# Kernel tuning notes

Measured on AMD Instinct MI355X. Metric: run time of the kernel, lower is better.

Reference implementation:

```python
import jax, jax.numpy as jnp
import numpy as np

B, S, HID = 4, 1024, 4096
NH, NKV, HD = 32, 8, 128
FF = 11008
EPS = 1e-6
THETA = 10000.0


def rms_norm(x, w, eps=EPS):
    v = jnp.mean(jnp.square(x), axis=-1, keepdims=True)
    return x * jax.lax.rsqrt(v + eps) * w


def rotate_half(x):
    x1, x2 = jnp.split(x, 2, axis=-1)
    return jnp.concatenate([-x2, x1], axis=-1)


def rope_cos_sin(position_ids, head_dim=HD, theta=THETA):
    inv_freq = 1.0 / (theta ** (jnp.arange(0, head_dim, 2, dtype=jnp.float32) / head_dim))
    freqs = position_ids.astype(jnp.float32)[..., None] * inv_freq  # [B,S,HD/2]
    emb = jnp.concatenate([freqs, freqs], axis=-1)  # [B,S,HD]
    return jnp.cos(emb)[:, None, :, :], jnp.sin(emb)[:, None, :, :]  # [B,1,S,HD]


def setup_inputs() -> dict:
    key = jax.random.key(0)
    ks = jax.random.split(key, 9)
    sc = 0.02
    pos = jnp.tile(jnp.arange(S, dtype=jnp.int64 if jax.config.jax_enable_x64 else jnp.int32)[None, :], (B, 1))
    causal = jnp.tril(jnp.ones((S, S), dtype=bool))
    mask = jnp.where(causal, 0.0, -1e9).astype(jnp.float32)[None, None]  # [1,1,S,S]
    return {
        "hidden_states": jax.random.normal(ks[0], (B * S, HID), jnp.float32),
        "position_ids": pos,
        "attn_mask": mask,
        "Wq": jax.random.normal(ks[1], (HID, NH * HD), jnp.float32) * sc,
        "Wk": jax.random.normal(ks[2], (HID, NKV * HD), jnp.float32) * sc,
        "Wv": jax.random.normal(ks[3], (HID, NKV * HD), jnp.float32) * sc,
        "Wo": jax.random.normal(ks[4], (NH * HD, HID), jnp.float32) * sc,
        "ln1_w": jnp.ones((HID,), jnp.float32),
        "ln2_w": jnp.ones((HID,), jnp.float32),
        "w_gate": jax.random.normal(ks[5], (HID, FF), jnp.float32) * sc,
        "w_up": jax.random.normal(ks[6], (HID, FF), jnp.float32) * sc,
        "w_down": jax.random.normal(ks[7], (FF, HID), jnp.float32) * sc,
    }


def reference(hidden_states, position_ids, attn_mask, Wq, Wk, Wv, Wo, ln1_w, ln2_w, w_gate, w_up, w_down):
    residual = hidden_states
    h = rms_norm(hidden_states, ln1_w)

    # QKV projections on flat tokens, then reshape per train partition
    q = (h @ Wq).reshape(B, S, NH, HD).transpose(0, 2, 1, 3)     # [B,NH,S,HD]
    k = (h @ Wk).reshape(B, S, NKV, HD).transpose(0, 2, 1, 3)    # [B,NKV,S,HD]
    v = (h @ Wv).reshape(B, S, NKV, HD).transpose(0, 2, 1, 3)

    cos, sin = rope_cos_sin(position_ids)
    q = q * cos + rotate_half(q) * sin
    k = k * cos + rotate_half(k) * sin

    n_rep = NH // NKV
    k = jnp.repeat(k, n_rep, axis=1)  # [B,NH,S,HD]
    v = jnp.repeat(v, n_rep, axis=1)

    scores = jnp.einsum('bhqd,bhkd->bhqk', q, k) / np.sqrt(HD)
    scores = scores + attn_mask
    # softmax in fp32 as in the source
    probs = jax.nn.softmax(scores.astype(jnp.float32), axis=-1).astype(q.dtype)
    attn = jnp.einsum('bhqk,bhkd->bhqd', probs, v)               # [B,NH,S,HD]
    attn = attn.transpose(0, 2, 1, 3).reshape(B * S, NH * HD)
    h = attn @ Wo

    h = residual + h
    residual = h
    h2 = rms_norm(h, ln2_w)
    mlp = (jax.nn.silu(h2 @ w_gate) * (h2 @ w_up)) @ w_down
    return residual + mlp
```

## Files before the change

### kernel.cpp

```cpp
#include <hip/hip_runtime.h>

#define DEVINL __device__ __forceinline__

typedef unsigned short u16;
typedef __attribute__((ext_vector_type(8))) short bf16x8;
typedef __attribute__((ext_vector_type(4))) float f32x4;
typedef __attribute__((ext_vector_type(4))) unsigned short u16x4;


DEVINL float bf2f(u16 u) { union { unsigned i; float f; } x; x.i = ((unsigned)u) << 16; return x.f; }
DEVINL u16 f2bf(float f) {
  union { float f; unsigned i; } x; x.f = f;
  unsigned r = x.i + 0x7fffu + ((x.i >> 16) & 1u);
  return (u16)(r >> 16);
}

DEVINL void async16(u16* lds, const u16* g) {
  __builtin_amdgcn_global_load_lds((const __attribute__((address_space(1))) unsigned*)g,
                                   (__attribute__((address_space(3))) unsigned*)lds, 16, 0, 0);
}

__global__ __launch_bounds__(256) void conv_t(const float* __restrict__ in,
                                              u16* __restrict__ out, int K, int N) {
  __shared__ float tile[64][65];
  int k0 = blockIdx.y << 6, n0 = blockIdx.x << 6;
  int t = threadIdx.x;
  int r = t >> 4, c4 = (t & 15) << 2;
  #pragma unroll
  for (int it = 0; it < 4; it++) {
    int row = r + it*16;
    f32x4 v = *(const f32x4*)(in + (size_t)(k0 + row)*N + n0 + c4);
    tile[row][c4+0] = v[0]; tile[row][c4+1] = v[1];
    tile[row][c4+2] = v[2]; tile[row][c4+3] = v[3];
  }
  __syncthreads();
  #pragma unroll
  for (int it = 0; it < 4; it++) {
    int nrow = r + it*16;
    u16x4 ov;
    #pragma unroll
    for (int e = 0; e < 4; e++) ov[e] = f2bf(tile[c4+e][nrow]);
    *(u16x4*)(out + (size_t)(n0 + nrow)*K + k0 + c4) = ov;
  }
}

__global__ __launch_bounds__(256) void rmsnorm_kernel(const float* __restrict__ x,
                                                      const float* __restrict__ w,
                                                      u16* __restrict__ out) {
  int row = blockIdx.x, t = threadIdx.x;
  const float* xr = x + (size_t)row * 4096;
  f32x4 v[4];
  float ss = 0.f;
  #pragma unroll
  for (int i = 0; i < 4; i++) {
    v[i] = *(const f32x4*)(xr + (t + 256*i)*4);
    ss += v[i][0]*v[i][0] + v[i][1]*v[i][1] + v[i][2]*v[i][2] + v[i][3]*v[i][3];
  }
  #pragma unroll
  for (int d = 1; d < 64; d <<= 1) ss += __shfl_xor(ss, d, 64);
  __shared__ float ps[4];
  if ((t & 63) == 0) ps[t >> 6] = ss;
  __syncthreads();
  float scale = rsqrtf((ps[0]+ps[1]+ps[2]+ps[3]) * (1.f/4096.f) + 1e-6f);
  #pragma unroll
  for (int i = 0; i < 4; i++) {
    f32x4 wv = *(const f32x4*)(w + (t + 256*i)*4);
    u16x4 o;
    #pragma unroll
    for (int e = 0; e < 4; e++) o[e] = f2bf(v[i][e] * scale * wv[e]);
    *(u16x4*)(out + (size_t)row*4096 + (t + 256*i)*4) = o;
  }
}

__global__ __launch_bounds__(256) void rope_kernel(u16* __restrict__ q, u16* __restrict__ k) {
  int tok = blockIdx.x;
  int s = tok & 1023;
  __shared__ float cs[64], sn[64];
  int t = threadIdx.x;
  if (t < 64) {
    float inv = __expf(-(float)t * 0.14391156934f);
    float ang = (float)s * inv;
    cs[t] = cosf(ang); sn[t] = sinf(ang);
  }
  __syncthreads();
  const float qscale = 0.08838834764831845f;
  size_t qbase = (size_t)tok * 4096;
  #pragma unroll
  for (int it = 0; it < 8; it++) {
    int item = t + it*256; int h = item >> 6, j = item & 63;
    size_t i0 = qbase + h*128 + j;
    float x1 = bf2f(q[i0]), x2 = bf2f(q[i0+64]);
    float c = cs[j], si = sn[j];
    q[i0]    = f2bf((x1*c - x2*si) * qscale);
    q[i0+64] = f2bf((x2*c + x1*si) * qscale);
  }
  size_t kbase = (size_t)tok * 1024;
  #pragma unroll
  for (int it = 0; it < 2; it++) {
    int item = t + it*256; int h = item >> 6, j = item & 63;
    size_t i0 = kbase + h*128 + j;
    float x1 = bf2f(k[i0]), x2 = bf2f(k[i0+64]);
    float c = cs[j], si = sn[j];
    k[i0]    = f2bf(x1*c - x2*si);
    k[i0+64] = f2bf(x2*c + x1*si);
  }
}

__global__ __launch_bounds__(256) void vtrans(const u16* __restrict__ v, u16* __restrict__ vt) {
  __shared__ u16 tile[32][33];
  int bh = blockIdx.z; int b = bh >> 3, kvh = bh & 7;
  int d0 = blockIdx.x << 5, s0 = blockIdx.y << 5;
  int tx = threadIdx.x, ty = threadIdx.y;
  for (int r = ty; r < 32; r += 8)
    tile[r][tx] = v[(size_t)(b*1024 + s0 + r)*1024 + kvh*128 + d0 + tx];
  __syncthreads();
  for (int r = ty; r < 32; r += 8)
    vt[(size_t)((b*8 + kvh)*128 + d0 + r)*1024 + s0 + tx] = tile[tx][r];
}

template<int EPI>
__global__ __launch_bounds__(256, 2) void gemm_bt(
    const u16* __restrict__ A, const u16* __restrict__ Bt,
    void* __restrict__ Cv, const float* __restrict__ resid,
    const u16* __restrict__ gate, int M, int N, int K) {
  __shared__ u16 As[128*64];
  __shared__ u16 Bs[128*64];
  int nwg = gridDim.x;
  int bid = (int)blockIdx.x;
  int cpx = nwg >> 3;
  int swz = (bid & 7) * cpx + (bid >> 3);
  int mt = M >> 7;
  int m0 = (swz % mt) << 7;
  int n0 = (swz / mt) << 7;
  int tid = threadIdx.x;
  int lane = tid & 63, wave = tid >> 6;
  int wm = wave >> 1, wn = wave & 1;

  f32x4 acc[4][4];
  f32x4 zero = {0.f, 0.f, 0.f, 0.f};
  #pragma unroll
  for (int i = 0; i < 4; i++)
    #pragma unroll
    for (int j = 0; j < 4; j++) acc[i][j] = zero;

  int arow[4], acolb[4];
  #pragma unroll
  for (int i = 0; i < 4; i++) {
    int c = i*256 + tid;
    arow[i]  = c >> 3;
    acolb[i] = ((c & 7) * 16) ^ ((arow[i] & 7) << 4);
  }

  int nsteps = K >> 6;
  for (int t = 0; t < nsteps; t++) {
    int k0 = t << 6;
    #pragma unroll
    for (int i = 0; i < 4; i++) {
      async16(As + i*2048 + wave*512, A  + (size_t)(m0 + arow[i])*K + k0 + (acolb[i] >> 1));
      async16(Bs + i*2048 + wave*512, Bt + (size_t)(n0 + arow[i])*K + k0 + (acolb[i] >> 1));
    }
    __syncthreads();
    #pragma unroll
    for (int ks = 0; ks < 2; ks++) {
      bf16x8 af[4], bfr[4];
      int c2 = (ks*32 + (lane >> 4)*8) * 2;
      #pragma unroll
      for (int mf = 0; mf < 4; mf++) {
        int r = wm*64 + mf*16 + (lane & 15);
        af[mf] = *(const bf16x8*)(As + r*64 + ((c2 ^ ((r & 7) << 4)) >> 1));
      }
      #pragma unroll
      for (int nf = 0; nf < 4; nf++) {
        int r = wn*64 + nf*16 + (lane & 15);
        bfr[nf] = *(const bf16x8*)(Bs + r*64 + ((c2 ^ ((r & 7) << 4)) >> 1));
      }
      #pragma unroll
      for (int mf = 0; mf < 4; mf++)
        #pragma unroll
        for (int nf = 0; nf < 4; nf++)
          acc[mf][nf] = __builtin_amdgcn_mfma_f32_16x16x32_bf16(af[mf], bfr[nf], acc[mf][nf], 0, 0, 0);
    }
    __syncthreads();
  }

  #pragma unroll
  for (int mf = 0; mf < 4; mf++)
    #pragma unroll
    for (int nf = 0; nf < 4; nf++)
      #pragma unroll
      for (int j = 0; j < 4; j++) {
        int rr = m0 + wm*64 + mf*16 + (lane >> 4)*4 + j;
        int cc = n0 + wn*64 + nf*16 + (lane & 15);
        size_t idx = (size_t)rr * N + cc;
        float v = acc[mf][nf][j];
        if constexpr (EPI == 0) {
          ((u16*)Cv)[idx] = f2bf(v);
        } else if constexpr (EPI == 1) {
          ((float*)Cv)[idx] = v + resid[idx];
        } else {
          float g = bf2f(gate[idx]);
          float sg = g / (1.f + __expf(-g));
          ((u16*)Cv)[idx] = f2bf(sg * v);
        }
      }
}

#define SB0() __builtin_amdgcn_sched_barrier(0)
#define MIDBAR() do { SB0(); __builtin_amdgcn_s_barrier(); \
  asm volatile("s_waitcnt lgkmcnt(0)" ::: "memory"); SB0(); } while (0)
#define MFMAQ2(qm, qn, afr, bq) do { \
  __builtin_amdgcn_s_setprio(1); \
  _Pragma("unroll") for (int mf_ = 0; mf_ < 4; mf_++) \
  _Pragma("unroll") for (int nf_ = 0; nf_ < 2; nf_++) \
  _Pragma("unroll") for (int ks_ = 0; ks_ < 2; ks_++) \
    acc[(qm)*4+mf_][(qn)*2+nf_] = __builtin_amdgcn_mfma_f32_16x16x32_bf16( \
        afr[mf_][ks_], bq[nf_][ks_], acc[(qm)*4+mf_][(qn)*2+nf_], 0, 0, 0); \
  __builtin_amdgcn_s_setprio(0); } while (0)

template<int EPI>
__global__ __launch_bounds__(512, 2) void gemm256(
    const u16* __restrict__ A, const u16* __restrict__ Bt,
    void* __restrict__ Cv, const float* __restrict__ resid,
    const u16* __restrict__ gate, int M, int N, int K) {
  extern __shared__ u16 lds[];
  int nwg = gridDim.x, bid = (int)blockIdx.x;
  int cpx = nwg >> 3;
  int swz = (bid & 7) * cpx + (bid >> 3);
  int mt = M >> 8;
  int m0 = (swz % mt) << 8;
  int n0 = (swz / mt) << 8;
  int tid = threadIdx.x, lane = tid & 63, wave = tid >> 6;
  int wm = wave >> 2, wn = wave & 3;

  f32x4 acc[8][4];
  f32x4 zero = {0.f, 0.f, 0.f, 0.f};
  #pragma unroll
  for (int i = 0; i < 8; i++)
    #pragma unroll
    for (int j = 0; j < 4; j++) acc[i][j] = zero;

  int sCol = ((lane & 7) ^ (lane >> 3)) << 3;
  int aRow = ((wave >> 2)*128) + (wave & 3)*16 + (lane >> 3);
  int bRow = ((wave >> 1)*64)  + (wave & 1)*16 + (lane >> 3);
  const u16* gA = A  + (size_t)(m0 + aRow) * K + sCol;
  const u16* gB = Bt + (size_t)(n0 + bRow) * K + sCol;
  size_t K8 = (size_t)8 * K, K32 = (size_t)32 * K, K64 = (size_t)64 * K;

  int rA = lane & 15;
  int acol0 = (((lane >> 4)    ) ^ (rA & 7)) << 3;
  int acol1 = (((lane >> 4) + 4) ^ (rA & 7)) << 3;

  bf16x8 af[4][2], b0[2][2], b1[2][2];

  auto stageAq = [&](int buf, int qm, int k0) {
    u16* d = lds + buf*32768 + qm*8192 + wave*1024;
    const u16* s = gA + (size_t)qm*K64 + k0;
    async16(d, s); async16(d + 512, s + K8);
  };
  auto stageBq = [&](int buf, int qn, int k0) {
    u16* d = lds + buf*32768 + 16384 + qn*8192 + wave*1024;
    const u16* s = gB + (size_t)qn*K32 + k0;
    async16(d, s); async16(d + 512, s + K8);
  };
  auto loadAq = [&](int buf, int qm) {
    const u16* base = lds + buf*32768 + qm*8192 + wm*4096 + rA*64;
    #pragma unroll
    for (int mf = 0; mf < 4; mf++) {
      af[mf][0] = *(const bf16x8*)(base + mf*1024 + acol0);
      af[mf][1] = *(const bf16x8*)(base + mf*1024 + acol1);
    }
  };
  auto loadBq = [&](int buf, int qn, bf16x8 (&bq)[2][2]) {
    const u16* base = lds + buf*32768 + 16384 + qn*8192 + wn*2048 + rA*64;
    #pragma unroll
    for (int nf = 0; nf < 2; nf++) {
      bq[nf][0] = *(const bf16x8*)(base + nf*1024 + acol0);
      bq[nf][1] = *(const bf16x8*)(base + nf*1024 + acol1);
    }
  };

  int nt = K >> 6;
  stageAq(0, 0, 0); stageBq(0, 0, 0); stageBq(0, 1, 0); stageAq(0, 1, 0);
  SB0();
  asm volatile("s_waitcnt vmcnt(4)" ::: "memory");
  SB0();
  __builtin_amdgcn_s_barrier();

  for (int k = 0; k < nt; k++) {
    int buf = k & 1, nbuf = buf ^ 1;
    bool pre = (k + 1) < nt;
    int k1 = (k + 1) << 6;
    loadAq(buf, 0); loadBq(buf, 0, b0);
    if (pre) stageAq(nbuf, 0, k1);
    MIDBAR();
    MFMAQ2(0, 0, af, b0);
    SB0();
    if (pre) asm volatile("s_waitcnt vmcnt(4)" ::: "memory");
    else     asm volatile("s_waitcnt vmcnt(2)" ::: "memory");
    SB0(); __builtin_amdgcn_s_barrier();
    loadBq(buf, 1, b1);
    if (pre) stageBq(nbuf, 0, k1);
    MIDBAR();
    MFMAQ2(0, 1, af, b1);
    SB0();
    if (pre) asm volatile("s_waitcnt vmcnt(4)" ::: "memory");
    else     asm volatile("s_waitcnt vmcnt(0)" ::: "memory");
    SB0(); __builtin_amdgcn_s_barrier();
    loadAq(buf, 1);
    if (pre) stageBq(nbuf, 1, k1);
    MIDBAR();
    MFMAQ2(1, 0, af, b0);
    SB0(); __builtin_amdgcn_s_barrier();
    if (pre) stageAq(nbuf, 1, k1);
    MIDBAR();
    MFMAQ2(1, 1, af, b1);
    SB0();
    if (pre) asm volatile("s_waitcnt vmcnt(4)" ::: "memory");
    SB0(); __builtin_amdgcn_s_barrier();
  }

  #pragma unroll
  for (int mf = 0; mf < 8; mf++)
    #pragma unroll
    for (int nf = 0; nf < 4; nf++)
      #pragma unroll
      for (int j = 0; j < 4; j++) {
        int rr = m0 + wm*128 + mf*16 + (lane >> 4)*4 + j;
        int cc = n0 + wn*64 + nf*16 + (lane & 15);
        size_t idx = (size_t)rr * N + cc;
        float v = acc[mf][nf][j];
        if constexpr (EPI == 0) {
          ((u16*)Cv)[idx] = f2bf(v);
        } else if constexpr (EPI == 1) {
          ((float*)Cv)[idx] = v + resid[idx];
        } else {
          float g = bf2f(gate[idx]);
          float sg = g / (1.f + __expf(-g));
          ((u16*)Cv)[idx] = f2bf(sg * v);
        }
      }
}

__global__ __launch_bounds__(256, 2) void attn_kernel(
    const u16* __restrict__ q, const u16* __restrict__ k,
    const u16* __restrict__ vt, u16* __restrict__ out) {
  __shared__ u16 Ks[64*128];
  __shared__ u16 Vs[128*64];
  __shared__ u16 Ps[4*16*64];
  int bid = blockIdx.x;
  int qt = bid & 15;
  int h  = (bid >> 4) & 31;
  int b  = bid >> 9;
  int kvh = h >> 2;
  int tid = threadIdx.x, lane = tid & 63, wave = tid >> 6;
  int q0 = qt << 6;

  bf16x8 qf[4];
  {
    const u16* qb_ = q + (size_t)(b*1024 + q0 + wave*16 + (lane & 15))*4096 + h*128 + (lane >> 4)*8;
    #pragma unroll
    for (int ks = 0; ks < 4; ks++) qf[ks] = *(const bf16x8*)(qb_ + ks*32);
  }
  f32x4 o[8];
  f32x4 zero = {0.f,0.f,0.f,0.f};
  #pragma unroll
  for (int i = 0; i < 8; i++) o[i] = zero;
  float m[4] = {-1e30f,-1e30f,-1e30f,-1e30f};
  float l[4] = {0.f,0.f,0.f,0.f};

  int kr[4], kc[4], vr[4], vc[4];
  #pragma unroll
  for (int i = 0; i < 4; i++) {
    int c = i*256 + tid;
    kr[i] = c >> 4; kc[i] = ((c & 15)*16) ^ ((kr[i] & 7) << 4);
    vr[i] = c >> 3; vc[i] = ((c & 7)*16)  ^ ((vr[i] & 7) << 4);
  }

  for (int t = 0; t <= qt; t++) {
    int kv0 = t << 6;
    #pragma unroll
    for (int i = 0; i < 4; i++) {
      async16(Ks + i*2048 + wave*512, k  + (size_t)(b*1024 + kv0 + kr[i])*1024 + kvh*128 + (kc[i] >> 1));
      async16(Vs + i*2048 + wave*512, vt + (size_t)((b*8 + kvh)*128 + vr[i])*1024 + kv0 + (vc[i] >> 1));
    }
    __syncthreads();

    f32x4 s[4];
    #pragma unroll
    for (int nf = 0; nf < 4; nf++) {
      s[nf] = zero;
      #pragma unroll
      for (int ks = 0; ks < 4; ks++) {
        int r = nf*16 + (lane & 15);
        int c2 = (ks*32 + (lane >> 4)*8)*2;
        bf16x8 kf = *(const bf16x8*)(Ks + r*128 + ((c2 ^ ((r & 7) << 4)) >> 1));
        s[nf] = __builtin_amdgcn_mfma_f32_16x16x32_bf16(qf[ks], kf, s[nf], 0, 0, 0);
      }
    }
    if (t == qt) {
      #pragma unroll
      for (int nf = 0; nf < 4; nf++)
        #pragma unroll
        for (int j = 0; j < 4; j++) {
          int cc = nf*16 + (lane & 15);
          int rr = wave*16 + (lane >> 4)*4 + j;
          if (cc > rr) s[nf][j] = -1e30f;
        }
    }
    #pragma unroll
    for (int j = 0; j < 4; j++) {
      float mx = fmaxf(fmaxf(s[0][j], s[1][j]), fmaxf(s[2][j], s[3][j]));
      #pragma unroll
      for (int d = 1; d < 16; d <<= 1) mx = fmaxf(mx, __shfl_xor(mx, d, 64));
      float mn = fmaxf(m[j], mx);
      float f = __expf(m[j] - mn);
      m[j] = mn;
      float ssum = 0.f;
      #pragma unroll
      for (int nf = 0; nf < 4; nf++) {
        float p = __expf(s[nf][j] - mn);
        s[nf][j] = p; ssum += p;
      }
      #pragma unroll
      for (int d = 1; d < 16; d <<= 1) ssum += __shfl_xor(ssum, d, 64);
      l[j] = l[j]*f + ssum;
      #pragma unroll
      for (int nf = 0; nf < 8; nf++) o[nf][j] *= f;
    }
    #pragma unroll
    for (int nf = 0; nf < 4; nf++)
      #pragma unroll
      for (int j = 0; j < 4; j++) {
        int rr = (lane >> 4)*4 + j;
        int cb = ((nf*16 + (lane & 15))*2) ^ ((rr & 7) << 4);
        Ps[wave*1024 + rr*64 + (cb >> 1)] = f2bf(s[nf][j]);
      }
    #pragma unroll
    for (int ks2 = 0; ks2 < 2; ks2++) {
      int mr = lane & 15;
      int c2 = (ks2*32 + (lane >> 4)*8)*2;
      bf16x8 pa = *(const bf16x8*)(Ps + wave*1024 + mr*64 + ((c2 ^ ((mr & 7) << 4)) >> 1));
      #pragma unroll
      for (int nf = 0; nf < 8; nf++) {
        int d = nf*16 + (lane & 15);
        bf16x8 vf = *(const bf16x8*)(Vs + d*64 + ((c2 ^ ((d & 7) << 4)) >> 1));
        o[nf] = __builtin_amdgcn_mfma_f32_16x16x32_bf16(pa, vf, o[nf], 0, 0, 0);
      }
    }
    __syncthreads();
  }

  float inv[4];
  #pragma unroll
  for (int j = 0; j < 4; j++) inv[j] = 1.f / l[j];
  u16* ob = out + (size_t)(b*1024 + q0 + wave*16)*4096 + h*128;
  #pragma unroll
  for (int nf = 0; nf < 8; nf++)
    #pragma unroll
    for (int j = 0; j < 4; j++) {
      int rr = (lane >> 4)*4 + j;
      int cc = nf*16 + (lane & 15);
      ob[(size_t)rr*4096 + cc] = f2bf(o[nf][j] * inv[j]);
    }
}

extern "C" void kernel_launch(void* const* d_in, const int* in_sizes, int n_in,
                              void* d_out, int out_size, void* d_ws, size_t ws_size,
                              hipStream_t stream) {
  (void)in_sizes; (void)n_in; (void)out_size;
  const float* hidden = (const float*)d_in[0];
  const float* Wq  = (const float*)d_in[3];
  const float* Wk  = (const float*)d_in[4];
  const float* Wv  = (const float*)d_in[5];
  const float* Wo  = (const float*)d_in[6];
  const float* ln1 = (const float*)d_in[7];
  const float* ln2 = (const float*)d_in[8];
  const float* Wg  = (const float*)d_in[9];
  const float* Wu  = (const float*)d_in[10];
  const float* Wd  = (const float*)d_in[11];
  float* out = (float*)d_out;

  char* ws = (char*)d_ws;
  size_t off = 0;
  auto alloc = [&](size_t b) { char* p = ws + off; off += (b + 4095) & ~(size_t)4095; return p; };
  u16*  W1   = (u16*)alloc(90177536);
  u16*  h1   = (u16*)alloc(33554432);
  u16*  qb   = (u16*)alloc(33554432);
  u16*  kb   = (u16*)alloc(8388608);
  u16*  vb   = (u16*)alloc(8388608);
  u16*  vtb  = (u16*)alloc(8388608);
  float* hmid = (float*)alloc(67108864);
  u16*  gb   = (u16*)alloc(90177536);
  if (off > ws_size) return;

  u16* wqT = W1;
  u16* wkT = W1 + 16777216;
  u16* wvT = wkT + 4194304;

  hipFuncSetAttribute((const void*)gemm256<0>, hipFuncAttributeMaxDynamicSharedMemorySize, 131072);
  hipFuncSetAttribute((const void*)gemm256<1>, hipFuncAttributeMaxDynamicSharedMemorySize, 131072);
  hipFuncSetAttribute((const void*)gemm256<2>, hipFuncAttributeMaxDynamicSharedMemorySize, 131072);

  dim3 blk(256);
  conv_t<<<dim3(64, 64),  blk, 0, stream>>>(Wq, wqT, 4096, 4096);
  conv_t<<<dim3(16, 64),  blk, 0, stream>>>(Wk, wkT, 4096, 1024);
  conv_t<<<dim3(16, 64),  blk, 0, stream>>>(Wv, wvT, 4096, 1024);
  rmsnorm_kernel<<<4096, blk, 0, stream>>>(hidden, ln1, h1);
  gemm256<0><<<256, 512, 131072, stream>>>(h1, wqT, qb, nullptr, nullptr, 4096, 4096, 4096);
  gemm_bt<0><<<256, blk, 0, stream>>>(h1, wkT, kb, nullptr, nullptr, 4096, 1024, 4096);
  gemm_bt<0><<<256, blk, 0, stream>>>(h1, wvT, vb, nullptr, nullptr, 4096, 1024, 4096);
  rope_kernel<<<4096, blk, 0, stream>>>(qb, kb);
  vtrans<<<dim3(4, 32, 32), dim3(32, 8), 0, stream>>>(vb, vtb);
  attn_kernel<<<2048, blk, 0, stream>>>(qb, kb, vtb, h1);
  conv_t<<<dim3(64, 64), blk, 0, stream>>>(Wo, W1, 4096, 4096);
  gemm256<1><<<256, 512, 131072, stream>>>(h1, W1, hmid, hidden, nullptr, 4096, 4096, 4096);
  rmsnorm_kernel<<<4096, blk, 0, stream>>>(hmid, ln2, qb);
  conv_t<<<dim3(172, 64), blk, 0, stream>>>(Wg, W1, 4096, 11008);
  gemm256<0><<<688, 512, 131072, stream>>>(qb, W1, gb, nullptr, nullptr, 4096, 11008, 4096);
  conv_t<<<dim3(172, 64), blk, 0, stream>>>(Wu, W1, 4096, 11008);
  gemm256<2><<<688, 512, 131072, stream>>>(qb, W1, gb, nullptr, gb, 4096, 11008, 4096);
  conv_t<<<dim3(64, 172), blk, 0, stream>>>(Wd, W1, 11008, 4096);
  gemm256<1><<<256, 512, 131072, stream>>>(gb, W1, out, hmid, nullptr, 4096, 4096, 11008);
}
```

Baseline: 1.836 ms.

## Overlap LDS fragment loads with MFMA via double-buffered A registers in gemm256

Restructures the 256x256 GEMM main loop so LDS-to-register fragment loads for the next quadrant (and the next K-tile's first A/B quadrant) are issued before the current MFMA block. Partial lgkmcnt waits replace the full lgkmcnt(0) after each barrier. A second A-fragment register set is added so loads and math can overlap, and two barriers per iteration are dropped. This aims to hide LDS read latency behind matrix-core work. The cost is more register pressure under launch_bounds(512,2) and fragile hand-counted wait counts.

After: 1.819 ms. About the same (-0.9%).

```diff
diff --git a/kernel.cpp b/kernel.cpp
--- a/kernel.cpp
+++ b/kernel.cpp
@@ -206,15 +206,13 @@
 }
 
 #define SB0() __builtin_amdgcn_sched_barrier(0)
-#define MIDBAR() do { SB0(); __builtin_amdgcn_s_barrier(); \
-  asm volatile("s_waitcnt lgkmcnt(0)" ::: "memory"); SB0(); } while (0)
-#define MFMAQ2(qm, qn, afr, bq) do { \
+#define MFMAQ2(qm, qn, AF, BQ) do { \
   __builtin_amdgcn_s_setprio(1); \
   _Pragma("unroll") for (int mf_ = 0; mf_ < 4; mf_++) \
   _Pragma("unroll") for (int nf_ = 0; nf_ < 2; nf_++) \
   _Pragma("unroll") for (int ks_ = 0; ks_ < 2; ks_++) \
     acc[(qm)*4+mf_][(qn)*2+nf_] = __builtin_amdgcn_mfma_f32_16x16x32_bf16( \
-        afr[mf_][ks_], bq[nf_][ks_], acc[(qm)*4+mf_][(qn)*2+nf_], 0, 0, 0); \
+        AF[mf_][ks_], BQ[nf_][ks_], acc[(qm)*4+mf_][(qn)*2+nf_], 0, 0, 0); \
   __builtin_amdgcn_s_setprio(0); } while (0)
 
 template<int EPI>
@@ -250,7 +248,7 @@
   int acol0 = (((lane >> 4)    ) ^ (rA & 7)) << 3;
   int acol1 = (((lane >> 4) + 4) ^ (rA & 7)) << 3;
 
-  bf16x8 af[4][2], b0[2][2], b1[2][2];
+  bf16x8 afA[4][2], afB[4][2], b0[2][2], b1[2][2];
 
   auto stageAq = [&](int buf, int qm, int k0) {
     u16* d = lds + buf*32768 + qm*8192 + wave*1024;
@@ -262,7 +260,7 @@
     const u16* s = gB + (size_t)qn*K32 + k0;
     async16(d, s); async16(d + 512, s + K8);
   };
-  auto loadAq = [&](int buf, int qm) {
+  auto loadAq = [&](int buf, int qm, bf16x8 (&af)[4][2]) {
     const u16* base = lds + buf*32768 + qm*8192 + wm*4096 + rA*64;
     #pragma unroll
     for (int mf = 0; mf < 4; mf++) {
@@ -282,41 +280,62 @@
   int nt = K >> 6;
   stageAq(0, 0, 0); stageBq(0, 0, 0); stageBq(0, 1, 0); stageAq(0, 1, 0);
   SB0();
-  asm volatile("s_waitcnt vmcnt(4)" ::: "memory");
+  asm volatile("s_waitcnt vmcnt(0)" ::: "memory");
   SB0();
   __builtin_amdgcn_s_barrier();
+  SB0();
+  loadAq(0, 0, afA); loadBq(0, 0, b0);
 
   for (int k = 0; k < nt; k++) {
     int buf = k & 1, nbuf = buf ^ 1;
     bool pre = (k + 1) < nt;
     int k1 = (k + 1) << 6;
-    loadAq(buf, 0); loadBq(buf, 0, b0);
-    if (pre) stageAq(nbuf, 0, k1);
-    MIDBAR();
-    MFMAQ2(0, 0, af, b0);
-    SB0();
-    if (pre) asm volatile("s_waitcnt vmcnt(4)" ::: "memory");
-    else     asm volatile("s_waitcnt vmcnt(2)" ::: "memory");
-    SB0(); __builtin_amdgcn_s_barrier();
+    if (pre) { stageAq(nbuf, 0, k1); SB0();
+               asm volatile("s_waitcnt vmcnt(4)" ::: "memory"); }
+    else     { asm volatile("s_waitcnt vmcnt(2)" ::: "memory"); }
+    SB0();
+    __builtin_amdgcn_s_barrier();
+    SB0();
     loadBq(buf, 1, b1);
-    if (pre) stageBq(nbuf, 0, k1);
-    MIDBAR();
-    MFMAQ2(0, 1, af, b1);
-    SB0();
-    if (pre) asm volatile("s_waitcnt vmcnt(4)" ::: "memory");
-    else     asm volatile("s_waitcnt vmcnt(0)" ::: "memory");
-    SB0(); __builtin_amdgcn_s_barrier();
-    loadAq(buf, 1);
-    if (pre) stageBq(nbuf, 1, k1);
-    MIDBAR();
-    MFMAQ2(1, 0, af, b0);
-    SB0(); __builtin_amdgcn_s_barrier();
-    if (pre) stageAq(nbuf, 1, k1);
-    MIDBAR();
-    MFMAQ2(1, 1, af, b1);
-    SB0();
-    if (pre) asm volatile("s_waitcnt vmcnt(4)" ::: "memory");
-    SB0(); __builtin_amdgcn_s_barrier();
+    asm volatile("s_waitcnt lgkmcnt(4)" ::: "memory");
+    SB0();
+    MFMAQ2(0, 0, afA, b0);
+    if (pre) { stageBq(nbuf, 0, k1); SB0();
+               asm volatile("s_waitcnt vmcnt(4)" ::: "memory"); }
+    else     { asm volatile("s_waitcnt vmcnt(0)" ::: "memory"); }
+    SB0();
+    __builtin_amdgcn_s_barrier();
+    SB0();
+    loadAq(buf, 1, afB);
+    asm volatile("s_waitcnt lgkmcnt(8)" ::: "memory");
+    SB0();
+    MFMAQ2(0, 1, afA, b1);
+    if (pre) { stageBq(nbuf, 1, k1); SB0();
+               asm volatile("s_waitcnt vmcnt(4)" ::: "memory"); }
+    SB0();
+    __builtin_amdgcn_s_barrier();
+    SB0();
+    if (pre) {
+      loadAq(nbuf, 0, afA);
+      asm volatile("s_waitcnt lgkmcnt(8)" ::: "memory");
+    } else {
+      asm volatile("s_waitcnt lgkmcnt(0)" ::: "memory");
+    }
+    SB0();
+    MFMAQ2(1, 0, afB, b0);
+    if (pre) { stageAq(nbuf, 1, k1); SB0();
+               asm volatile("s_waitcnt vmcnt(4)" ::: "memory"); }
+    SB0();
+    __builtin_amdgcn_s_barrier();
+    SB0();
+    if (pre) {
+      loadBq(nbuf, 0, b0);
+      asm volatile("s_waitcnt lgkmcnt(12)" ::: "memory");
+    } else {
+      asm volatile("s_waitcnt lgkmcnt(0)" ::: "memory");
+    }
+    SB0();
+    MFMAQ2(1, 1, afB, b1);
   }
 
   #pragma unroll
```

## Overlap weight conversions with attention/GEMM blocks and deepen GEMM K pipeline

Applied to the files above, without the earlier changes.

Weight transpose-convert jobs are merged into one launch or appended as extra blocks to the attention and up-projection GEMM kernels, so the conversion runs alongside compute instead of as separate serialized launches. Separate workspace buffers per weight make this possible, at the cost of more workspace (with a fallback path when it is too small). The GEMM main loop is rewritten with a compile-time K, two k-steps per iteration, double A fragment registers and staged prefetch two tiles ahead. This raises register pressure and adds scheduling complexity.

After: 1.698 ms. -7.5%, faster.

```diff
diff --git a/kernel.cpp b/kernel.cpp
--- a/kernel.cpp
+++ b/kernel.cpp
@@ -20,18 +20,20 @@
                                    (__attribute__((address_space(3))) unsigned*)lds, 16, 0, 0);
 }
 
-__global__ __launch_bounds__(256) void conv_t(const float* __restrict__ in,
-                                              u16* __restrict__ out, int K, int N) {
-  __shared__ float tile[64][65];
-  int k0 = blockIdx.y << 6, n0 = blockIdx.x << 6;
-  int t = threadIdx.x;
+struct CJob { const float* in; u16* out; int K, N, ntiles; };
+
+DEVINL void conv_one(const float* __restrict__ in, u16* __restrict__ out,
+                     int K, int N, int tile, int t, float (*tl)[65]) {
+  int tn = N >> 6;
+  int kt = tile / tn;
+  int k0 = kt << 6, n0 = (tile - kt*tn) << 6;
   int r = t >> 4, c4 = (t & 15) << 2;
   #pragma unroll
   for (int it = 0; it < 4; it++) {
     int row = r + it*16;
     f32x4 v = *(const f32x4*)(in + (size_t)(k0 + row)*N + n0 + c4);
-    tile[row][c4+0] = v[0]; tile[row][c4+1] = v[1];
-    tile[row][c4+2] = v[2]; tile[row][c4+3] = v[3];
+    tl[row][c4+0] = v[0]; tl[row][c4+1] = v[1];
+    tl[row][c4+2] = v[2]; tl[row][c4+3] = v[3];
   }
   __syncthreads();
   #pragma unroll
@@ -39,9 +41,29 @@
     int nrow = r + it*16;
     u16x4 ov;
     #pragma unroll
-    for (int e = 0; e < 4; e++) ov[e] = f2bf(tile[c4+e][nrow]);
+    for (int e = 0; e < 4; e++) ov[e] = f2bf(tl[c4+e][nrow]);
     *(u16x4*)(out + (size_t)(n0 + nrow)*K + k0 + c4) = ov;
   }
+  __syncthreads();
+}
+
+__global__ __launch_bounds__(256) void conv3(CJob j0, CJob j1, CJob j2) {
+  __shared__ float tl[64][65];
+  int ntot = j0.ntiles + j1.ntiles + j2.ntiles;
+  for (int g = blockIdx.x; g < ntot; g += gridDim.x) {
+    const float* in; u16* out; int K, N, tile;
+    if (g < j0.ntiles)                 { in = j0.in; out = j0.out; K = j0.K; N = j0.N; tile = g; }
+    else if (g < j0.ntiles + j1.ntiles){ in = j1.in; out = j1.out; K = j1.K; N = j1.N; tile = g - j0.ntiles; }
+    else                               { in = j2.in; out = j2.out; K = j2.K; N = j2.N; tile = g - j0.ntiles - j1.ntiles; }
+    conv_one(in, out, K, N, tile, threadIdx.x, tl);
+  }
+}
+
+__global__ __launch_bounds__(256) void conv_t(const float* __restrict__ in,
+                                              u16* __restrict__ out, int K, int N) {
+  __shared__ float tl[64][65];
+  int tile = blockIdx.y * gridDim.x + blockIdx.x;
+  conv_one(in, out, K, N, tile, threadIdx.x, tl);
 }
 
 __global__ __launch_bounds__(256) void rmsnorm_kernel(const float* __restrict__ x,
@@ -206,30 +228,44 @@
 }
 
 #define SB0() __builtin_amdgcn_sched_barrier(0)
-#define MIDBAR() do { SB0(); __builtin_amdgcn_s_barrier(); \
-  asm volatile("s_waitcnt lgkmcnt(0)" ::: "memory"); SB0(); } while (0)
-#define MFMAQ2(qm, qn, afr, bq) do { \
+#define BAR() __builtin_amdgcn_s_barrier()
+#define LGKM(n) do { SB0(); asm volatile("s_waitcnt lgkmcnt(" #n ")" ::: "memory"); SB0(); } while (0)
+#define VMC(n)  do { SB0(); asm volatile("s_waitcnt vmcnt(" #n ")"  ::: "memory"); SB0(); } while (0)
+#define MFMAQ(qm, qn, AF, BQ) do { \
   __builtin_amdgcn_s_setprio(1); \
   _Pragma("unroll") for (int mf_ = 0; mf_ < 4; mf_++) \
   _Pragma("unroll") for (int nf_ = 0; nf_ < 2; nf_++) \
   _Pragma("unroll") for (int ks_ = 0; ks_ < 2; ks_++) \
     acc[(qm)*4+mf_][(qn)*2+nf_] = __builtin_amdgcn_mfma_f32_16x16x32_bf16( \
-        afr[mf_][ks_], bq[nf_][ks_], acc[(qm)*4+mf_][(qn)*2+nf_], 0, 0, 0); \
+        AF[mf_][ks_], BQ[nf_][ks_], acc[(qm)*4+mf_][(qn)*2+nf_], 0, 0, 0); \
   __builtin_amdgcn_s_setprio(0); } while (0)
 
-template<int EPI>
+template<int KC, int EPI>
 __global__ __launch_bounds__(512, 2) void gemm256(
     const u16* __restrict__ A, const u16* __restrict__ Bt,
     void* __restrict__ Cv, const float* __restrict__ resid,
-    const u16* __restrict__ gate, int M, int N, int K) {
+    const u16* __restrict__ gate, int M, int N, int G,
+    const float* __restrict__ cvin, u16* __restrict__ cvout, int cvK, int cvN, int cvTiles) {
   extern __shared__ u16 lds[];
-  int nwg = gridDim.x, bid = (int)blockIdx.x;
-  int cpx = nwg >> 3;
+  int bid = (int)blockIdx.x;
+  int tid = threadIdx.x;
+
+  if (bid >= G) {
+    int cb = bid - G, CB = (int)gridDim.x - G;
+    int h = tid >> 8, t = tid & 255;
+    float (*tl)[65] = (float(*)[65])((char*)lds + h*16896);
+    int pairs = cvTiles >> 1;
+    for (int p = cb; p < pairs; p += CB)
+      conv_one(cvin, cvout, cvK, cvN, 2*p + h, t, tl);
+    return;
+  }
+
+  int cpx = G >> 3;
   int swz = (bid & 7) * cpx + (bid >> 3);
   int mt = M >> 8;
   int m0 = (swz % mt) << 8;
   int n0 = (swz / mt) << 8;
-  int tid = threadIdx.x, lane = tid & 63, wave = tid >> 6;
+  int lane = tid & 63, wave = tid >> 6;
   int wm = wave >> 2, wn = wave & 3;
 
   f32x4 acc[8][4];
@@ -240,17 +276,17 @@
     for (int j = 0; j < 4; j++) acc[i][j] = zero;
 
   int sCol = ((lane & 7) ^ (lane >> 3)) << 3;
-  int aRow = ((wave >> 2)*128) + (wave & 3)*16 + (lane >> 3);
-  int bRow = ((wave >> 1)*64)  + (wave & 1)*16 + (lane >> 3);
-  const u16* gA = A  + (size_t)(m0 + aRow) * K + sCol;
-  const u16* gB = Bt + (size_t)(n0 + bRow) * K + sCol;
-  size_t K8 = (size_t)8 * K, K32 = (size_t)32 * K, K64 = (size_t)64 * K;
+  int aRow = (wave >> 2)*128 + (wave & 3)*16 + (lane >> 3);
+  int bRow = (wave >> 1)*64  + (wave & 1)*16 + (lane >> 3);
+  const u16* gA = A  + (size_t)(m0 + aRow) * KC + sCol;
+  const u16* gB = Bt + (size_t)(n0 + bRow) * KC + sCol;
+  constexpr size_t K8 = (size_t)8 * KC, K32 = (size_t)32 * KC, K64 = (size_t)64 * KC;
 
   int rA = lane & 15;
   int acol0 = (((lane >> 4)    ) ^ (rA & 7)) << 3;
   int acol1 = (((lane >> 4) + 4) ^ (rA & 7)) << 3;
 
-  bf16x8 af[4][2], b0[2][2], b1[2][2];
+  bf16x8 afA[4][2], afB[4][2], b0[2][2], b1[2][2];
 
   auto stageAq = [&](int buf, int qm, int k0) {
     u16* d = lds + buf*32768 + qm*8192 + wave*1024;
@@ -262,7 +298,7 @@
     const u16* s = gB + (size_t)qn*K32 + k0;
     async16(d, s); async16(d + 512, s + K8);
   };
-  auto loadAq = [&](int buf, int qm) {
+  auto loadAq = [&](int buf, int qm, bf16x8 (&af)[4][2]) {
     const u16* base = lds + buf*32768 + qm*8192 + wm*4096 + rA*64;
     #pragma unroll
     for (int mf = 0; mf < 4; mf++) {
@@ -279,44 +315,75 @@
     }
   };
 
-  int nt = K >> 6;
+  constexpr int nt = KC >> 6;
+  constexpr int IT = nt/2 - 1;
+
   stageAq(0, 0, 0); stageBq(0, 0, 0); stageBq(0, 1, 0); stageAq(0, 1, 0);
-  SB0();
-  asm volatile("s_waitcnt vmcnt(4)" ::: "memory");
-  SB0();
-  __builtin_amdgcn_s_barrier();
-
-  for (int k = 0; k < nt; k++) {
-    int buf = k & 1, nbuf = buf ^ 1;
-    bool pre = (k + 1) < nt;
-    int k1 = (k + 1) << 6;
-    loadAq(buf, 0); loadBq(buf, 0, b0);
-    if (pre) stageAq(nbuf, 0, k1);
-    MIDBAR();
-    MFMAQ2(0, 0, af, b0);
-    SB0();
-    if (pre) asm volatile("s_waitcnt vmcnt(4)" ::: "memory");
-    else     asm volatile("s_waitcnt vmcnt(2)" ::: "memory");
-    SB0(); __builtin_amdgcn_s_barrier();
-    loadBq(buf, 1, b1);
-    if (pre) stageBq(nbuf, 0, k1);
-    MIDBAR();
-    MFMAQ2(0, 1, af, b1);
-    SB0();
-    if (pre) asm volatile("s_waitcnt vmcnt(4)" ::: "memory");
-    else     asm volatile("s_waitcnt vmcnt(0)" ::: "memory");
-    SB0(); __builtin_amdgcn_s_barrier();
-    loadAq(buf, 1);
-    if (pre) stageBq(nbuf, 1, k1);
-    MIDBAR();
-    MFMAQ2(1, 0, af, b0);
-    SB0(); __builtin_amdgcn_s_barrier();
-    if (pre) stageAq(nbuf, 1, k1);
-    MIDBAR();
-    MFMAQ2(1, 1, af, b1);
-    SB0();
-    if (pre) asm volatile("s_waitcnt vmcnt(4)" ::: "memory");
-    SB0(); __builtin_amdgcn_s_barrier();
+  VMC(4);
+  stageAq(1, 0, 64); stageBq(1, 0, 64); stageBq(1, 1, 64);
+  VMC(6);
+  BAR();
+
+  #pragma unroll 1
+  for (int it = 0; it < IT; it++) {
+    int kc = it*128;
+    loadAq(0, 0, afA); loadBq(0, 0, b0); stageAq(1, 1, kc + 64);
+    LGKM(8); BAR(); LGKM(0);
+    MFMAQ(0, 0, afA, b0);
+    SB0(); BAR();
+    loadBq(0, 1, b1); stageAq(0, 0, kc + 128);
+    BAR(); LGKM(0);
+    MFMAQ(0, 1, afA, b1);
+    SB0(); BAR();
+    loadAq(0, 1, afB); stageBq(0, 0, kc + 128);
+    BAR(); LGKM(0);
+    MFMAQ(1, 0, afB, b0);
+    SB0(); BAR();
+    stageBq(0, 1, kc + 128);
+    BAR();
+    MFMAQ(1, 1, afB, b1);
+    VMC(6); BAR();
+    loadAq(1, 0, afA); loadBq(1, 0, b0); stageAq(0, 1, kc + 128);
+    LGKM(8); BAR(); LGKM(0);
+    MFMAQ(0, 0, afA, b0);
+    SB0(); BAR();
+    loadBq(1, 1, b1); stageAq(1, 0, kc + 192);
+    BAR(); LGKM(0);
+    MFMAQ(0, 1, afA, b1);
+    SB0(); BAR();
+    loadAq(1, 1, afB); stageBq(1, 0, kc + 192);
+    BAR(); LGKM(0);
+    MFMAQ(1, 0, afB, b0);
+    SB0(); BAR();
+    stageBq(1, 1, kc + 192);
+    BAR();
+    MFMAQ(1, 1, afB, b1);
+    VMC(6); BAR();
+  }
+
+  {
+    int kc = IT*128;
+    loadAq(0, 0, afA); loadBq(0, 0, b0); stageAq(1, 1, kc + 64);
+    LGKM(8); BAR(); LGKM(0);
+    MFMAQ(0, 0, afA, b0);
+    SB0(); BAR();
+    loadBq(0, 1, b1);
+    BAR(); LGKM(0);
+    MFMAQ(0, 1, afA, b1);
+    SB0(); BAR();
+    loadAq(0, 1, afB);
+    BAR(); LGKM(0);
+    MFMAQ(1, 0, afB, b0);
+    SB0(); BAR();
+    MFMAQ(1, 1, afB, b1);
+    VMC(0); BAR();
+    loadAq(1, 0, afA); loadBq(1, 0, b0); SB0();
+    loadBq(1, 1, b1); SB0();
+    loadAq(1, 1, afB); SB0();
+    LGKM(12); MFMAQ(0, 0, afA, b0);
+    LGKM(8);  MFMAQ(0, 1, afA, b1);
+    LGKM(0);  MFMAQ(1, 0, afB, b0);
+    MFMAQ(1, 1, afB, b1);
   }
 
   #pragma unroll
@@ -343,11 +410,28 @@
 
 __global__ __launch_bounds__(256, 2) void attn_kernel(
     const u16* __restrict__ q, const u16* __restrict__ k,
-    const u16* __restrict__ vt, u16* __restrict__ out) {
-  __shared__ u16 Ks[64*128];
-  __shared__ u16 Vs[128*64];
-  __shared__ u16 Ps[4*16*64];
+    const u16* __restrict__ vt, u16* __restrict__ out,
+    CJob j0, CJob j1, CJob j2) {
+  __shared__ __align__(16) u16 shm[20480];
+  u16* Ks = shm;
+  u16* Vs = shm + 8192;
+  u16* Ps = shm + 16384;
   int bid = blockIdx.x;
+
+  if (bid >= 2048) {
+    int cb = bid - 2048, CB = (int)gridDim.x - 2048;
+    float (*tl)[65] = (float(*)[65])shm;
+    int ntot = j0.ntiles + j1.ntiles + j2.ntiles;
+    for (int g = cb; g < ntot; g += CB) {
+      const float* in; u16* outp; int K, N, tile;
+      if (g < j0.ntiles)                  { in = j0.in; outp = j0.out; K = j0.K; N = j0.N; tile = g; }
+      else if (g < j0.ntiles + j1.ntiles) { in = j1.in; outp = j1.out; K = j1.K; N = j1.N; tile = g - j0.ntiles; }
+      else                                { in = j2.in; outp = j2.out; K = j2.K; N = j2.N; tile = g - j0.ntiles - j1.ntiles; }
+      conv_one(in, outp, K, N, tile, threadIdx.x, tl);
+    }
+    return;
+  }
+
   int qt = bid & 15;
   int h  = (bid >> 4) & 31;
   int b  = bid >> 9;
@@ -432,8 +516,8 @@
       #pragma unroll
       for (int j = 0; j < 4; j++) {
         int rr = (lane >> 4)*4 + j;
-        int cb = ((nf*16 + (lane & 15))*2) ^ ((rr & 7) << 4);
-        Ps[wave*1024 + rr*64 + (cb >> 1)] = f2bf(s[nf][j]);
+        int cb2 = ((nf*16 + (lane & 15))*2) ^ ((rr & 7) << 4);
+        Ps[wave*1024 + rr*64 + (cb2 >> 1)] = f2bf(s[nf][j]);
       }
     #pragma unroll
     for (int ks2 = 0; ks2 < 2; ks2++) {
@@ -480,45 +564,93 @@
   const float* Wd  = (const float*)d_in[11];
   float* out = (float*)d_out;
 
+  hipFuncSetAttribute((const void*)gemm256<4096,0>,  hipFuncAttributeMaxDynamicSharedMemorySize, 131072);
+  hipFuncSetAttribute((const void*)gemm256<4096,1>,  hipFuncAttributeMaxDynamicSharedMemorySize, 131072);
+  hipFuncSetAttribute((const void*)gemm256<4096,2>,  hipFuncAttributeMaxDynamicSharedMemorySize, 131072);
+  hipFuncSetAttribute((const void*)gemm256<11008,1>, hipFuncAttributeMaxDynamicSharedMemorySize, 131072);
+
   char* ws = (char*)d_ws;
   size_t off = 0;
   auto alloc = [&](size_t b) { char* p = ws + off; off += (b + 4095) & ~(size_t)4095; return p; };
-  u16*  W1   = (u16*)alloc(90177536);
-  u16*  h1   = (u16*)alloc(33554432);
-  u16*  qb   = (u16*)alloc(33554432);
-  u16*  kb   = (u16*)alloc(8388608);
-  u16*  vb   = (u16*)alloc(8388608);
-  u16*  vtb  = (u16*)alloc(8388608);
+
+  u16*  wqkvT = (u16*)alloc(50331648);
+  u16*  woT   = (u16*)alloc(33554432);
+  u16*  wgT   = (u16*)alloc(90177536);
+  u16*  wuT   = (u16*)alloc(90177536);
+  u16*  h1    = (u16*)alloc(33554432);
+  u16*  qb    = (u16*)alloc(33554432);
+  u16*  kb    = (u16*)alloc(8388608);
+  u16*  vb    = (u16*)alloc(8388608);
+  u16*  vtb   = (u16*)alloc(8388608);
   float* hmid = (float*)alloc(67108864);
-  u16*  gb   = (u16*)alloc(90177536);
-  if (off > ws_size) return;
-
-  u16* wqT = W1;
-  u16* wkT = W1 + 16777216;
-  u16* wvT = wkT + 4194304;
-
-  hipFuncSetAttribute((const void*)gemm256<0>, hipFuncAttributeMaxDynamicSharedMemorySize, 131072);
-  hipFuncSetAttribute((const void*)gemm256<1>, hipFuncAttributeMaxDynamicSharedMemorySize, 131072);
-  hipFuncSetAttribute((const void*)gemm256<2>, hipFuncAttributeMaxDynamicSharedMemorySize, 131072);
+  u16*  gb    = (u16*)alloc(90177536);
+  bool fused = off <= ws_size;
 
   dim3 blk(256);
-  conv_t<<<dim3(64, 64),  blk, 0, stream>>>(Wq, wqT, 4096, 4096);
-  conv_t<<<dim3(16, 64),  blk, 0, stream>>>(Wk, wkT, 4096, 1024);
-  conv_t<<<dim3(16, 64),  blk, 0, stream>>>(Wv, wvT, 4096, 1024);
-  rmsnorm_kernel<<<4096, blk, 0, stream>>>(hidden, ln1, h1);
-  gemm256<0><<<256, 512, 131072, stream>>>(h1, wqT, qb, nullptr, nullptr, 4096, 4096, 4096);
-  gemm_bt<0><<<256, blk, 0, stream>>>(h1, wkT, kb, nullptr, nullptr, 4096, 1024, 4096);
-  gemm_bt<0><<<256, blk, 0, stream>>>(h1, wvT, vb, nullptr, nullptr, 4096, 1024, 4096);
-  rope_kernel<<<4096, blk, 0, stream>>>(qb, kb);
-  vtrans<<<dim3(4, 32, 32), dim3(32, 8), 0, stream>>>(vb, vtb);
-  attn_kernel<<<2048, blk, 0, stream>>>(qb, kb, vtb, h1);
-  conv_t<<<dim3(64, 64), blk, 0, stream>>>(Wo, W1, 4096, 4096);
-  gemm256<1><<<256, 512, 131072, stream>>>(h1, W1, hmid, hidden, nullptr, 4096, 4096, 4096);
-  rmsnorm_kernel<<<4096, blk, 0, stream>>>(hmid, ln2, qb);
-  conv_t<<<dim3(172, 64), blk, 0, stream>>>(Wg, W1, 4096, 11008);
-  gemm256<0><<<688, 512, 131072, stream>>>(qb, W1, gb, nullptr, nullptr, 4096, 11008, 4096);
-  conv_t<<<dim3(172, 64), blk, 0, stream>>>(Wu, W1, 4096, 11008);
-  gemm256<2><<<688, 512, 131072, stream>>>(qb, W1, gb, nullptr, gb, 4096, 11008, 4096);
-  conv_t<<<dim3(64, 172), blk, 0, stream>>>(Wd, W1, 11008, 4096);
-  gemm256<1><<<256, 512, 131072, stream>>>(gb, W1, out, hmid, nullptr, 4096, 4096, 11008);
-}
+  if (fused) {
+    u16* wqT = wqkvT;
+    u16* wkT = wqkvT + 16777216;
+    u16* wvT = wkT + 4194304;
+    u16* wdT = wgT;
+    CJob Jq{Wq, wqT, 4096, 4096, 4096}, Jk{Wk, wkT, 4096, 1024, 1024}, Jv{Wv, wvT, 4096, 1024, 1024};
+    CJob Jo{Wo, woT, 4096, 4096, 4096}, Jg{Wg, wgT, 4096, 11008, 11008}, Ju{Wu, wuT, 4096, 11008, 11008};
+
+    conv3<<<2048, blk, 0, stream>>>(Jq, Jk, Jv);
+    rmsnorm_kernel<<<4096, blk, 0, stream>>>(hidden, ln1, h1);
+    gemm256<4096,0><<<256, 512, 131072, stream>>>(h1, wqT, qb, nullptr, nullptr, 4096, 4096, 256,
+                                                  nullptr, nullptr, 0, 0, 0);
+    gemm_bt<0><<<256, blk, 0, stream>>>(h1, wkT, kb, nullptr, nullptr, 4096, 1024, 4096);
+    gemm_bt<0><<<256, blk, 0, stream>>>(h1, wvT, vb, nullptr, nullptr, 4096, 1024, 4096);
+    rope_kernel<<<4096, blk, 0, stream>>>(qb, kb);
+    vtrans<<<dim3(4, 32, 32), dim3(32, 8), 0, stream>>>(vb, vtb);
+    attn_kernel<<<2048 + 1024, blk, 0, stream>>>(qb, kb, vtb, h1, Jo, Jg, Ju);
+    gemm256<4096,1><<<256, 512, 131072, stream>>>(h1, woT, hmid, hidden, nullptr, 4096, 4096, 256,
+                                                  nullptr, nullptr, 0, 0, 0);
+    rmsnorm_kernel<<<4096, blk, 0, stream>>>(hmid, ln2, qb);
+    gemm256<4096,0><<<688, 512, 131072, stream>>>(qb, wgT, gb, nullptr, nullptr, 4096, 11008, 688,
+                                                  nullptr, nullptr, 0, 0, 0);
+    gemm256<4096,2><<<688 + 344, 512, 131072, stream>>>(qb, wuT, gb, nullptr, gb, 4096, 11008, 688,
+                                                        Wd, wdT, 11008, 4096, 11008);
+    gemm256<11008,1><<<256, 512, 131072, stream>>>(gb, wdT, out, hmid, nullptr, 4096, 4096, 256,
+                                                   nullptr, nullptr, 0, 0, 0);
+  } else {
+    off = 0;
+    u16*  W1   = (u16*)alloc(90177536);
+    u16*  h1s  = (u16*)alloc(33554432);
+    u16*  qbs  = (u16*)alloc(33554432);
+    u16*  kbs  = (u16*)alloc(8388608);
+    u16*  vbs  = (u16*)alloc(8388608);
+    u16*  vtbs = (u16*)alloc(8388608);
+    float* hmids = (float*)alloc(67108864);
+    u16*  gbs  = (u16*)alloc(90177536);
+    if (off > ws_size) return;
+    u16* wqT = W1;
+    u16* wkT = W1 + 16777216;
+    u16* wvT = wkT + 4194304;
+    conv_t<<<dim3(64, 64),  blk, 0, stream>>>(Wq, wqT, 4096, 4096);
+    conv_t<<<dim3(16, 64),  blk, 0, stream>>>(Wk, wkT, 4096, 1024);
+    conv_t<<<dim3(16, 64),  blk, 0, stream>>>(Wv, wvT, 4096, 1024);
+    rmsnorm_kernel<<<4096, blk, 0, stream>>>(hidden, ln1, h1s);
+    gemm256<4096,0><<<256, 512, 131072, stream>>>(h1s, wqT, qbs, nullptr, nullptr, 4096, 4096, 256,
+                                                  nullptr, nullptr, 0, 0, 0);
+    gemm_bt<0><<<256, blk, 0, stream>>>(h1s, wkT, kbs, nullptr, nullptr, 4096, 1024, 4096);
+    gemm_bt<0><<<256, blk, 0, stream>>>(h1s, wvT, vbs, nullptr, nullptr, 4096, 1024, 4096);
+    rope_kernel<<<4096, blk, 0, stream>>>(qbs, kbs);
+    vtrans<<<dim3(4, 32, 32), dim3(32, 8), 0, stream>>>(vbs, vtbs);
+    CJob J0{nullptr, nullptr, 0, 64, 0};
+    attn_kernel<<<2048, blk, 0, stream>>>(qbs, kbs, vtbs, h1s, J0, J0, J0);
+    conv_t<<<dim3(64, 64), blk, 0, stream>>>(Wo, W1, 4096, 4096);
+    gemm256<4096,1><<<256, 512, 131072, stream>>>(h1s, W1, hmids, hidden, nullptr, 4096, 4096, 256,
+                                                  nullptr, nullptr, 0, 0, 0);
+    rmsnorm_kernel<<<4096, blk, 0, stream>>>(hmids, ln2, qbs);
+    conv_t<<<dim3(172, 64), blk, 0, stream>>>(Wg, W1, 4096, 11008);
+    gemm256<4096,0><<<688, 512, 131072, stream>>>(qbs, W1, gbs, nullptr, nullptr, 4096, 11008, 688,
+                                                  nullptr, nullptr, 0, 0, 0);
+    conv_t<<<dim3(172, 64), blk, 0, stream>>>(Wu, W1, 4096, 11008);
+    gemm256<4096,2><<<688, 512, 131072, stream>>>(qbs, W1, gbs, nullptr, gbs, 4096, 11008, 688,
+                                                  nullptr, nullptr, 0, 0, 0);
+    conv_t<<<dim3(64, 172), blk, 0, stream>>>(Wd, W1, 11008, 4096);
+    gemm256<11008,1><<<256, 512, 131072, stream>>>(gbs, W1, out, hmids, nullptr, 4096, 4096, 256,
+                                                   nullptr, nullptr, 0, 0, 0);
+  }
+}
```
